# Performance work log

Hardware: AMD Instinct MI355X
Metric: run time of the kernel (lower is better)

## Reference

```python
import jax, jax.numpy as jnp
import numpy as np

DIM = 1024
D_STATE = 16
D_CONV = 4
EXPAND = 2
D_INNER = EXPAND * DIM
BATCH = 4
SEQ = 2048


def setup_inputs() -> dict:
    key = jax.random.key(0)
    ks = jax.random.split(key, 9)
    n = lambda i, shape, scale=0.02: (jax.random.normal(ks[i], shape, jnp.float32) * scale)
    return {
        "x": jax.random.normal(ks[0], (BATCH, SEQ, DIM), jnp.float32),
        "in_proj_w": n(1, (D_INNER, DIM)),
        "conv_w": n(2, (D_INNER, D_CONV), 0.1),          # depthwise kernel (groups=d_inner)
        "x_proj_w": n(3, (2 * D_STATE + 1, D_INNER)),
        "dt_proj_w": n(4, (D_INNER, 1), 1.0),
        "dt_proj_b": n(5, (D_INNER,), 0.1),
        "A_log": jax.random.normal(ks[6], (D_INNER, D_STATE), jnp.float32),
        "D": jnp.ones((D_INNER,), jnp.float32),
        "out_proj_w": n(7, (DIM, D_INNER)),
        "norm_w": jnp.ones((DIM,), jnp.float32),
        "norm_b": jnp.zeros((DIM,), jnp.float32),
    }


def reference(x, in_proj_w, conv_w, x_proj_w, dt_proj_w, dt_proj_b,
              A_log, D, out_proj_w, norm_w, norm_b):
    Bsz, L, _ = x.shape
    shortcut = x

    # LayerNorm
    mu = jnp.mean(x, axis=-1, keepdims=True)
    var = jnp.var(x, axis=-1, keepdims=True)
    h = (x - mu) / jnp.sqrt(var + 1e-5) * norm_w + norm_b

    # in_proj: [B,L,dim] -> [B,L,d_inner]
    h = h @ in_proj_w.T

    # causal depthwise conv1d (padding d_conv-1, truncate to L)
    hp = jnp.pad(h, ((0, 0), (D_CONV - 1, 0), (0, 0)))
    h_conv = sum(hp[:, k:k + L, :] * conv_w[:, k] for k in range(D_CONV))
    h = jax.nn.silu(h_conv)

    # x_proj -> dt (1), B (d_state), C (d_state)
    proj = h @ x_proj_w.T
    dt_in = proj[..., :1]
    B_param = proj[..., 1:1 + D_STATE]      # [B,L,d_state]
    C_param = proj[..., 1 + D_STATE:]       # [B,L,d_state]
    dt = jax.nn.softplus(dt_in @ dt_proj_w.T + dt_proj_b)  # [B,L,d_inner]

    A = -jnp.exp(A_log)                     # [d_inner, d_state]

    def step(state, inp):
        dt_t, B_t, C_t, x_t = inp           # [B,d_inner],[B,ds],[B,ds],[B,d_inner]
        state = jnp.exp(A[None] * dt_t[:, :, None]) * state \
                + B_t[:, None, :] * x_t[:, :, None]          # [B,d_inner,d_state]
        y = jnp.einsum('bnd,bd->bn', state, C_t) + D * x_t   # [B,d_inner]
        return state, y

    init = jnp.zeros((Bsz, D_INNER, D_STATE), x.dtype)
    xs = (jnp.swapaxes(dt, 0, 1), jnp.swapaxes(B_param, 0, 1),
          jnp.swapaxes(C_param, 0, 1), jnp.swapaxes(h, 0, 1))
    state, ys = jax.lax.scan(step, init, xs)
    y = jnp.swapaxes(ys, 0, 1)              # [B,L,d_inner]

    out = jax.nn.silu(y) @ out_proj_w.T + shortcut
    return out, state
```

## Files before the change

kernel.cpp:

```cpp
#include <hip/hip_runtime.h>

typedef unsigned short u16;
typedef unsigned int u32;
typedef __attribute__((ext_vector_type(8))) short short8;
typedef __attribute__((ext_vector_type(4))) float f32x4;
typedef __attribute__((ext_vector_type(8))) unsigned short ushort8_t;

#define SEQ 2048
#define DIM 1024
#define DINNER 2048
#define NPROJ 33
#define NPROJ_PAD 48
#define LC 64
#define NC 32

__device__ __forceinline__ u16 f2bf(float f) {
  union { float f; u32 u; } v; v.f = f;
  u32 r = (v.u + 0x7fffu + ((v.u >> 16) & 1u)) >> 16;
  return (u16)r;
}
__device__ __forceinline__ float bf2f(u16 s) {
  union { u32 u; float f; } v; v.u = ((u32)s) << 16;
  return v.f;
}
__device__ __forceinline__ float fexp2(float x) {
#if __has_builtin(__builtin_amdgcn_exp2f)
  return __builtin_amdgcn_exp2f(x);
#else
  return __expf(x * 0.69314718f);
#endif
}
__device__ __forceinline__ float softplus(float x) {
  return fmaxf(x, 0.f) + __logf(1.f + __expf(-fabsf(x)));
}
__device__ __forceinline__ void async16(const void* g, void* l) {
  __builtin_amdgcn_global_load_lds(
      (const __attribute__((address_space(1))) u32*)g,
      (__attribute__((address_space(3))) u32*)l, 16, 0, 0);
}

__global__ void cast_f2b_kernel(const float* __restrict__ src, u16* __restrict__ dst, int n4) {
  int i = blockIdx.x * 256 + threadIdx.x;
  if (i < n4) {
    float4 v = ((const float4*)src)[i];
    ushort4 o;
    o.x = f2bf(v.x); o.y = f2bf(v.y); o.z = f2bf(v.z); o.w = f2bf(v.w);
    ((ushort4*)dst)[i] = o;
  }
}

__global__ void cast_w2pad_kernel(const float* __restrict__ src, u16* __restrict__ dst) {
  int i = blockIdx.x * 256 + threadIdx.x;
  int j = i >> 11, k = i & 2047;
  dst[i] = (j < NPROJ) ? f2bf(src[j * 2048 + k]) : (u16)0;
}

__global__ __launch_bounds__(256) void ln_kernel(const float* __restrict__ x,
                                                 const float* __restrict__ w,
                                                 const float* __restrict__ b,
                                                 u16* __restrict__ h) {
  const int row = blockIdx.x;
  const int tid = threadIdx.x;
  const int lane = tid & 63, wave = tid >> 6;
  const float4 v = ((const float4*)(x + (size_t)row * DIM))[tid];
  float s = v.x + v.y + v.z + v.w;
  float q = v.x * v.x + v.y * v.y + v.z * v.z + v.w * v.w;
  for (int off = 32; off; off >>= 1) {
    s += __shfl_down(s, off);
    q += __shfl_down(q, off);
  }
  __shared__ float sbuf[8];
  if (lane == 0) { sbuf[wave] = s; sbuf[4 + wave] = q; }
  __syncthreads();
  float tot = sbuf[0] + sbuf[1] + sbuf[2] + sbuf[3];
  float totq = sbuf[4] + sbuf[5] + sbuf[6] + sbuf[7];
  const float mean = tot * (1.0f / DIM);
  const float var = totq * (1.0f / DIM) - mean * mean;
  const float rs = rsqrtf(var + 1e-5f);
  const float4 wv = ((const float4*)w)[tid];
  const float4 bv = ((const float4*)b)[tid];
  ushort4 o;
  o.x = f2bf((v.x - mean) * rs * wv.x + bv.x);
  o.y = f2bf((v.y - mean) * rs * wv.y + bv.y);
  o.z = f2bf((v.z - mean) * rs * wv.z + bv.z);
  o.w = f2bf((v.w - mean) * rs * wv.w + bv.w);
  ((ushort4*)(h + (size_t)row * DIM))[tid] = o;
}

__global__ __launch_bounds__(256) void gemm_bf16_kernel(const u16* __restrict__ A,
                                                        const u16* __restrict__ Bt,
                                                        u16* __restrict__ C,
                                                        int K, int N) {
  __shared__ u16 As[128 * 32];
  __shared__ u16 Bs[128 * 32];
  const int tid = threadIdx.x;
  const int lane = tid & 63, wave = tid >> 6;
  const int wm = wave >> 1, wn = wave & 1;
  const int row16 = lane & 15, quad = lane >> 4;
  const int bn = blockIdx.x, bm = blockIdx.y;
  f32x4 acc[4][4] = {};
  const u16* Ablk = A + (size_t)bm * 128 * K;
  const u16* Bblk = Bt + (size_t)bn * 128 * K;
  for (int k0 = 0; k0 < K; k0 += 32) {
#pragma unroll
    for (int i = 0; i < 2; ++i) {
      int c = tid + i * 256;
      int r = c >> 2, cc = (c & 3) * 8;
      async16(Ablk + (size_t)r * K + k0 + cc, &As[c * 8]);
      async16(Bblk + (size_t)r * K + k0 + cc, &Bs[c * 8]);
    }
    __syncthreads();
    short8 af[4], bfr[4];
#pragma unroll
    for (int i = 0; i < 4; ++i) {
      af[i] = *(const short8*)&As[(wm * 64 + i * 16 + row16) * 32 + quad * 8];
      bfr[i] = *(const short8*)&Bs[(wn * 64 + i * 16 + row16) * 32 + quad * 8];
    }
#pragma unroll
    for (int i = 0; i < 4; ++i)
#pragma unroll
      for (int j = 0; j < 4; ++j)
        acc[i][j] = __builtin_amdgcn_mfma_f32_16x16x32_bf16(af[i], bfr[j], acc[i][j], 0, 0, 0);
    __syncthreads();
  }
#pragma unroll
  for (int i = 0; i < 4; ++i) {
    int m = bm * 128 + wm * 64 + i * 16 + quad * 4;
#pragma unroll
    for (int j = 0; j < 4; ++j) {
      int n = bn * 128 + wn * 64 + j * 16 + row16;
#pragma unroll
      for (int r = 0; r < 4; ++r)
        C[(size_t)(m + r) * N + n] = f2bf(acc[i][j][r]);
    }
  }
}

__global__ __launch_bounds__(256) void gemm_out_kernel(const u16* __restrict__ A,
                                                       const u16* __restrict__ Bt,
                                                       const float* __restrict__ resid,
                                                       float* __restrict__ C,
                                                       int K, int N) {
  __shared__ u16 As[128 * 32];
  __shared__ u16 Bs[128 * 32];
  const int tid = threadIdx.x;
  const int lane = tid & 63, wave = tid >> 6;
  const int wm = wave >> 1, wn = wave & 1;
  const int row16 = lane & 15, quad = lane >> 4;
  const int bn = blockIdx.x, bm = blockIdx.y;
  f32x4 acc[4][4] = {};
  const u16* Ablk = A + (size_t)bm * 128 * K;
  const u16* Bblk = Bt + (size_t)bn * 128 * K;
  for (int k0 = 0; k0 < K; k0 += 32) {
#pragma unroll
    for (int i = 0; i < 2; ++i) {
      int c = tid + i * 256;
      int r = c >> 2, cc = (c & 3) * 8;
      async16(Ablk + (size_t)r * K + k0 + cc, &As[c * 8]);
      async16(Bblk + (size_t)r * K + k0 + cc, &Bs[c * 8]);
    }
    __syncthreads();
    short8 af[4], bfr[4];
#pragma unroll
    for (int i = 0; i < 4; ++i) {
      af[i] = *(const short8*)&As[(wm * 64 + i * 16 + row16) * 32 + quad * 8];
      bfr[i] = *(const short8*)&Bs[(wn * 64 + i * 16 + row16) * 32 + quad * 8];
    }
#pragma unroll
    for (int i = 0; i < 4; ++i)
#pragma unroll
      for (int j = 0; j < 4; ++j)
        acc[i][j] = __builtin_amdgcn_mfma_f32_16x16x32_bf16(af[i], bfr[j], acc[i][j], 0, 0, 0);
    __syncthreads();
  }
#pragma unroll
  for (int i = 0; i < 4; ++i) {
    int m = bm * 128 + wm * 64 + i * 16 + quad * 4;
#pragma unroll
    for (int j = 0; j < 4; ++j) {
      int n = bn * 128 + wn * 64 + j * 16 + row16;
#pragma unroll
      for (int r = 0; r < 4; ++r) {
        size_t idx = (size_t)(m + r) * N + n;
        C[idx] = acc[i][j][r] + resid[idx];
      }
    }
  }
}

__global__ __launch_bounds__(256) void conv_silu_kernel(const u16* __restrict__ c1,
                                                        const float* __restrict__ cw,
                                                        u16* __restrict__ cs) {
  const int tid = threadIdx.x;
  const int dg = tid * 8;
  const size_t m0 = (size_t)blockIdx.x * 8;
  const int l0 = (int)(m0 & (SEQ - 1));
  float w[4][8];
  {
    const float4* cw4 = (const float4*)(cw + (size_t)dg * 4);
#pragma unroll
    for (int c = 0; c < 8; ++c) {
      float4 v = cw4[c];
      w[0][c] = v.x; w[1][c] = v.y; w[2][c] = v.z; w[3][c] = v.w;
    }
  }
  const u16* base = c1 + m0 * DINNER + dg;
  ushort8_t win0, win1, win2, win3;
  const ushort8_t zero = (ushort8_t)0;
  if (l0 == 0) {
    win0 = zero; win1 = zero; win2 = zero;
  } else {
    win0 = *(const ushort8_t*)(base - 3 * DINNER);
    win1 = *(const ushort8_t*)(base - 2 * DINNER);
    win2 = *(const ushort8_t*)(base - 1 * DINNER);
  }
  win3 = *(const ushort8_t*)(base);
#pragma unroll
  for (int t = 0; t < 8; ++t) {
    ushort8_t nxt = win3;
    if (t < 7) nxt = *(const ushort8_t*)(base + (size_t)(t + 1) * DINNER);
    ushort8_t o;
#pragma unroll
    for (int c = 0; c < 8; ++c) {
      float acc = bf2f((u16)win0[c]) * w[0][c];
      acc = fmaf(bf2f((u16)win1[c]), w[1][c], acc);
      acc = fmaf(bf2f((u16)win2[c]), w[2][c], acc);
      acc = fmaf(bf2f((u16)win3[c]), w[3][c], acc);
      const float s = acc / (1.f + __expf(-acc));
      o[c] = (unsigned short)f2bf(s);
    }
    *(ushort8_t*)(cs + (m0 + t) * DINNER + dg) = o;
    win0 = win1; win1 = win2; win2 = win3; win3 = nxt;
  }
}

__global__ __launch_bounds__(256) void gemm_w2_kernel(const u16* __restrict__ A,
                                                      const u16* __restrict__ Bt,
                                                      float* __restrict__ C) {
  __shared__ u16 As[128 * 32];
  __shared__ u16 Bs[48 * 32];
  const int tid = threadIdx.x;
  const int lane = tid & 63, wave = tid >> 6;
  const int row16 = lane & 15, quad = lane >> 4;
  const int bm = blockIdx.x;
  const int K = DINNER;
  f32x4 acc[2][3] = {};
  const u16* Ablk = A + (size_t)bm * 128 * K;
  for (int k0 = 0; k0 < K; k0 += 32) {
#pragma unroll
    for (int i = 0; i < 2; ++i) {
      int c = tid + i * 256;
      int r = c >> 2, cc = (c & 3) * 8;
      async16(Ablk + (size_t)r * K + k0 + cc, &As[c * 8]);
    }
    if (tid < 192) {
      int c = tid;
      int r = c >> 2, cc = (c & 3) * 8;
      async16(Bt + (size_t)r * K + k0 + cc, &Bs[c * 8]);
    }
    __syncthreads();
    short8 af[2], bfr[3];
#pragma unroll
    for (int i = 0; i < 2; ++i)
      af[i] = *(const short8*)&As[(wave * 32 + i * 16 + row16) * 32 + quad * 8];
#pragma unroll
    for (int j = 0; j < 3; ++j)
      bfr[j] = *(const short8*)&Bs[(j * 16 + row16) * 32 + quad * 8];
#pragma unroll
    for (int i = 0; i < 2; ++i)
#pragma unroll
      for (int j = 0; j < 3; ++j)
        acc[i][j] = __builtin_amdgcn_mfma_f32_16x16x32_bf16(af[i], bfr[j], acc[i][j], 0, 0, 0);
    __syncthreads();
  }
#pragma unroll
  for (int i = 0; i < 2; ++i) {
    int m = bm * 128 + wave * 32 + i * 16 + quad * 4;
#pragma unroll
    for (int j = 0; j < 3; ++j) {
      int n = j * 16 + row16;
#pragma unroll
      for (int r = 0; r < 4; ++r)
        C[(size_t)(m + r) * NPROJ_PAD + n] = acc[i][j][r];
    }
  }
}

__global__ __launch_bounds__(256) void scan_phase1(const float* __restrict__ proj,
                                                   const u16* __restrict__ xs,
                                                   const float* __restrict__ dtw_,
                                                   const float* __restrict__ dtb_,
                                                   const float* __restrict__ A_log,
                                                   float* __restrict__ S,
                                                   float* __restrict__ Tdt) {
  __shared__ float Bs[LC][16];
  __shared__ float DTin[LC];
  const int tid = threadIdx.x;
  const int d = blockIdx.x * 256 + tid;
  const int c = blockIdx.y;
  const int b = blockIdx.z;
  const size_t mrow = (size_t)b * SEQ + c * LC;
  for (int i = tid; i < LC * 16; i += 256) {
    int t = i >> 4, n = i & 15;
    Bs[t][n] = proj[(mrow + t) * NPROJ_PAD + 1 + n];
  }
  if (tid < LC) DTin[tid] = proj[(mrow + tid) * NPROJ_PAD];
  __syncthreads();
  float An2[16];
#pragma unroll
  for (int n = 0; n < 16; ++n) An2[n] = -__expf(A_log[d * 16 + n]) * 1.44269504f;
  const float dtw = dtw_[d], dtb = dtb_[d];
  float s[16];
#pragma unroll
  for (int n = 0; n < 16; ++n) s[n] = 0.f;
  float Tsum = 0.f;
  const u16* xp = xs + mrow * DINNER + d;
  u16 xnext = *xp;
#pragma unroll 2
  for (int t = 0; t < LC; ++t) {
    const float xv = bf2f(xnext);
    if (t + 1 < LC) xnext = xp[(size_t)(t + 1) * DINNER];
    const float sp = softplus(fmaf(DTin[t], dtw, dtb));
    Tsum += sp;
    const float4 B0 = *(const float4*)&Bs[t][0];
    const float4 B1 = *(const float4*)&Bs[t][4];
    const float4 B2 = *(const float4*)&Bs[t][8];
    const float4 B3 = *(const float4*)&Bs[t][12];
    const float bb[16] = {B0.x, B0.y, B0.z, B0.w, B1.x, B1.y, B1.z, B1.w,
                          B2.x, B2.y, B2.z, B2.w, B3.x, B3.y, B3.z, B3.w};
#pragma unroll
    for (int n = 0; n < 16; ++n)
      s[n] = fmaf(fexp2(An2[n] * sp), s[n], bb[n] * xv);
  }
  const size_t so = ((size_t)(b * NC + c) * DINNER + d) * 16;
#pragma unroll
  for (int n4 = 0; n4 < 4; ++n4)
    *(float4*)(S + so + n4 * 4) = make_float4(s[n4 * 4], s[n4 * 4 + 1], s[n4 * 4 + 2], s[n4 * 4 + 3]);
  Tdt[(size_t)(b * NC + c) * DINNER + d] = Tsum;
}

__global__ __launch_bounds__(256) void scan_phase2(const float* __restrict__ A_log,
                                                   float* __restrict__ S,
                                                   const float* __restrict__ Tdt,
                                                   float* __restrict__ out_state) {
  const int idx = blockIdx.x * 256 + threadIdx.x;
  const int b = idx >> 11, d = idx & (DINNER - 1);
  float An2[16];
#pragma unroll
  for (int n = 0; n < 16; ++n) An2[n] = -__expf(A_log[d * 16 + n]) * 1.44269504f;
  float prev[16];
#pragma unroll
  for (int n = 0; n < 16; ++n) prev[n] = 0.f;
  for (int c = 0; c < NC; ++c) {
    const size_t so = ((size_t)(b * NC + c) * DINNER + d) * 16;
    const float T = Tdt[(size_t)(b * NC + c) * DINNER + d];
    float loc[16];
#pragma unroll
    for (int n4 = 0; n4 < 4; ++n4) {
      float4 v = *(const float4*)(S + so + n4 * 4);
      loc[n4 * 4] = v.x; loc[n4 * 4 + 1] = v.y; loc[n4 * 4 + 2] = v.z; loc[n4 * 4 + 3] = v.w;
    }
#pragma unroll
    for (int n4 = 0; n4 < 4; ++n4)
      *(float4*)(S + so + n4 * 4) =
          make_float4(prev[n4 * 4], prev[n4 * 4 + 1], prev[n4 * 4 + 2], prev[n4 * 4 + 3]);
#pragma unroll
    for (int n = 0; n < 16; ++n)
      prev[n] = fmaf(fexp2(An2[n] * T), prev[n], loc[n]);
  }
#pragma unroll
  for (int n4 = 0; n4 < 4; ++n4)
    *(float4*)(out_state + ((size_t)b * DINNER + d) * 16 + n4 * 4) =
        make_float4(prev[n4 * 4], prev[n4 * 4 + 1], prev[n4 * 4 + 2], prev[n4 * 4 + 3]);
}

__global__ __launch_bounds__(256) void scan_phase3(const float* __restrict__ proj,
                                                   const u16* __restrict__ xs,
                                                   const float* __restrict__ dtw_,
                                                   const float* __restrict__ dtb_,
                                                   const float* __restrict__ A_log,
                                                   const float* __restrict__ Dp,
                                                   const float* __restrict__ S,
                                                   u16* __restrict__ ysil) {
  __shared__ float Bs[LC][16];
  __shared__ float Cs[LC][16];
  __shared__ float DTin[LC];
  const int tid = threadIdx.x;
  const int d = blockIdx.x * 256 + tid;
  const int c = blockIdx.y;
  const int b = blockIdx.z;
  const size_t mrow = (size_t)b * SEQ + c * LC;
  for (int i = tid; i < LC * 16; i += 256) {
    int t = i >> 4, n = i & 15;
    Bs[t][n] = proj[(mrow + t) * NPROJ_PAD + 1 + n];
    Cs[t][n] = proj[(mrow + t) * NPROJ_PAD + 17 + n];
  }
  if (tid < LC) DTin[tid] = proj[(mrow + tid) * NPROJ_PAD];
  __syncthreads();
  float An2[16];
#pragma unroll
  for (int n = 0; n < 16; ++n) An2[n] = -__expf(A_log[d * 16 + n]) * 1.44269504f;
  const float dtw = dtw_[d], dtb = dtb_[d], Dd = Dp[d];
  float s[16];
  const size_t so = ((size_t)(b * NC + c) * DINNER + d) * 16;
#pragma unroll
  for (int n4 = 0; n4 < 4; ++n4) {
    float4 v = *(const float4*)(S + so + n4 * 4);
    s[n4 * 4] = v.x; s[n4 * 4 + 1] = v.y; s[n4 * 4 + 2] = v.z; s[n4 * 4 + 3] = v.w;
  }
  const u16* xp = xs + mrow * DINNER + d;
  u16* yp = ysil + mrow * DINNER + d;
  u16 xnext = *xp;
#pragma unroll 2
  for (int t = 0; t < LC; ++t) {
    const float xv = bf2f(xnext);
    if (t + 1 < LC) xnext = xp[(size_t)(t + 1) * DINNER];
    const float sp = softplus(fmaf(DTin[t], dtw, dtb));
    const float4 B0 = *(const float4*)&Bs[t][0];
    const float4 B1 = *(const float4*)&Bs[t][4];
    const float4 B2 = *(const float4*)&Bs[t][8];
    const float4 B3 = *(const float4*)&Bs[t][12];
    const float bb[16] = {B0.x, B0.y, B0.z, B0.w, B1.x, B1.y, B1.z, B1.w,
                          B2.x, B2.y, B2.z, B2.w, B3.x, B3.y, B3.z, B3.w};
#pragma unroll
    for (int n = 0; n < 16; ++n)
      s[n] = fmaf(fexp2(An2[n] * sp), s[n], bb[n] * xv);
    const float4 C0 = *(const float4*)&Cs[t][0];
    const float4 C1 = *(const float4*)&Cs[t][4];
    const float4 C2 = *(const float4*)&Cs[t][8];
    const float4 C3 = *(const float4*)&Cs[t][12];
    const float cc[16] = {C0.x, C0.y, C0.z, C0.w, C1.x, C1.y, C1.z, C1.w,
                          C2.x, C2.y, C2.z, C2.w, C3.x, C3.y, C3.z, C3.w};
    float y = Dd * xv;
#pragma unroll
    for (int n = 0; n < 16; ++n) y = fmaf(cc[n], s[n], y);
    const float sy = y / (1.f + __expf(-y));
    yp[(size_t)t * DINNER] = f2bf(sy);
  }
}

extern "C" void kernel_launch(void* const* d_in, const int* in_sizes, int n_in,
                              void* d_out, int out_size, void* d_ws, size_t ws_size,
                              hipStream_t stream) {
  const float* x = (const float*)d_in[0];
  const float* in_proj_w = (const float*)d_in[1];
  const float* conv_w = (const float*)d_in[2];
  const float* x_proj_w = (const float*)d_in[3];
  const float* dt_proj_w = (const float*)d_in[4];
  const float* dt_proj_b = (const float*)d_in[5];
  const float* A_log = (const float*)d_in[6];
  const float* Dvec = (const float*)d_in[7];
  const float* out_proj_w = (const float*)d_in[8];
  const float* norm_w = (const float*)d_in[9];
  const float* norm_b = (const float*)d_in[10];

  char* ws = (char*)d_ws;
  u16* h = (u16*)(ws + 0);
  u16* w1b = (u16*)(ws + 16777216);
  u16* w3b = (u16*)(ws + 20971520);
  u16* w2b = (u16*)(ws + 25165824);
  u16* c1 = (u16*)(ws + 25362432);
  u16* ysil = c1;
  u16* cs = (u16*)(ws + 58916864);
  float* proj = (float*)(ws + 92471296);
  float* Sbuf = (float*)(ws + 94044160);
  float* Tdt = (float*)(ws + 110821376);

  float* out = (float*)d_out;
  float* out_state = out + (size_t)4 * SEQ * DIM;

  cast_f2b_kernel<<<2048, 256, 0, stream>>>(in_proj_w, w1b, DINNER * DIM / 4);
  cast_f2b_kernel<<<2048, 256, 0, stream>>>(out_proj_w, w3b, DIM * DINNER / 4);
  cast_w2pad_kernel<<<384, 256, 0, stream>>>(x_proj_w, w2b);
  ln_kernel<<<8192, 256, 0, stream>>>(x, norm_w, norm_b, h);
  gemm_bf16_kernel<<<dim3(DINNER / 128, 64), 256, 0, stream>>>(h, w1b, c1, DIM, DINNER);
  conv_silu_kernel<<<1024, 256, 0, stream>>>(c1, conv_w, cs);
  gemm_w2_kernel<<<64, 256, 0, stream>>>(cs, w2b, proj);
  scan_phase1<<<dim3(DINNER / 256, NC, 4), 256, 0, stream>>>(proj, cs, dt_proj_w, dt_proj_b,
                                                             A_log, Sbuf, Tdt);
  scan_phase2<<<32, 256, 0, stream>>>(A_log, Sbuf, Tdt, out_state);
  scan_phase3<<<dim3(DINNER / 256, NC, 4), 256, 0, stream>>>(proj, cs, dt_proj_w, dt_proj_b,
                                                             A_log, Dvec, Sbuf, ysil);
  gemm_out_kernel<<<dim3(DIM / 128, 64), 256, 0, stream>>>(ysil, w3b, x, out, DINNER, DIM);
}
```

Measured before the change: 424.7 us.

## Halve scan chunk length, store chunk states in bf16, widen phase2, fuse weight casts

Scan chunks shrink from 64 to 32 steps, doubling chunk count so phases 1 and 3 run more blocks with shorter serial loops. Inter-chunk states are stored as bf16, halving S buffer traffic. Phase 2 is parallelised across state-dimension quarters, giving four times as many threads. The two weight-cast launches are merged into one. The bf16 state carry adds rounding error to the recurrence and the final state, and phase 2 now walks twice as many chunks serially.

```diff
diff --git a/kernel.cpp b/kernel.cpp
--- a/kernel.cpp
+++ b/kernel.cpp
@@ -11,8 +11,8 @@
 #define DINNER 2048
 #define NPROJ 33
 #define NPROJ_PAD 48
-#define LC 64
-#define NC 32
+#define LC 32
+#define NC 64
 
 __device__ __forceinline__ u16 f2bf(float f) {
   union { float f; u32 u; } v; v.f = f;
@@ -39,14 +39,16 @@
       (__attribute__((address_space(3))) u32*)l, 16, 0, 0);
 }
 
-__global__ void cast_f2b_kernel(const float* __restrict__ src, u16* __restrict__ dst, int n4) {
+__global__ void cast_w_kernel(const float* __restrict__ w1, const float* __restrict__ w3,
+                              u16* __restrict__ o1, u16* __restrict__ o3) {
   int i = blockIdx.x * 256 + threadIdx.x;
-  if (i < n4) {
-    float4 v = ((const float4*)src)[i];
-    ushort4 o;
-    o.x = f2bf(v.x); o.y = f2bf(v.y); o.z = f2bf(v.z); o.w = f2bf(v.w);
-    ((ushort4*)dst)[i] = o;
-  }
+  float4 a = ((const float4*)w1)[i];
+  float4 b = ((const float4*)w3)[i];
+  ushort4 oa, ob;
+  oa.x = f2bf(a.x); oa.y = f2bf(a.y); oa.z = f2bf(a.z); oa.w = f2bf(a.w);
+  ob.x = f2bf(b.x); ob.y = f2bf(b.y); ob.z = f2bf(b.z); ob.w = f2bf(b.w);
+  ((ushort4*)o1)[i] = oa;
+  ((ushort4*)o3)[i] = ob;
 }
 
 __global__ void cast_w2pad_kernel(const float* __restrict__ src, u16* __restrict__ dst) {
@@ -286,12 +288,13 @@
   }
 }
 
+
 __global__ __launch_bounds__(256) void scan_phase1(const float* __restrict__ proj,
                                                    const u16* __restrict__ xs,
                                                    const float* __restrict__ dtw_,
                                                    const float* __restrict__ dtb_,
                                                    const float* __restrict__ A_log,
-                                                   float* __restrict__ S,
+                                                   u16* __restrict__ S,
                                                    float* __restrict__ Tdt) {
   __shared__ float Bs[LC][16];
   __shared__ float DTin[LC];
@@ -333,45 +336,47 @@
       s[n] = fmaf(fexp2(An2[n] * sp), s[n], bb[n] * xv);
   }
   const size_t so = ((size_t)(b * NC + c) * DINNER + d) * 16;
-#pragma unroll
-  for (int n4 = 0; n4 < 4; ++n4)
-    *(float4*)(S + so + n4 * 4) = make_float4(s[n4 * 4], s[n4 * 4 + 1], s[n4 * 4 + 2], s[n4 * 4 + 3]);
+  ushort8_t o0, o1;
+#pragma unroll
+  for (int j = 0; j < 8; ++j) {
+    o0[j] = (unsigned short)f2bf(s[j]);
+    o1[j] = (unsigned short)f2bf(s[8 + j]);
+  }
+  *(ushort8_t*)(S + so) = o0;
+  *(ushort8_t*)(S + so + 8) = o1;
   Tdt[(size_t)(b * NC + c) * DINNER + d] = Tsum;
 }
 
 __global__ __launch_bounds__(256) void scan_phase2(const float* __restrict__ A_log,
-                                                   float* __restrict__ S,
+                                                   u16* __restrict__ S,
                                                    const float* __restrict__ Tdt,
                                                    float* __restrict__ out_state) {
   const int idx = blockIdx.x * 256 + threadIdx.x;
-  const int b = idx >> 11, d = idx & (DINNER - 1);
-  float An2[16];
-#pragma unroll
-  for (int n = 0; n < 16; ++n) An2[n] = -__expf(A_log[d * 16 + n]) * 1.44269504f;
-  float prev[16];
-#pragma unroll
-  for (int n = 0; n < 16; ++n) prev[n] = 0.f;
+  const int nq = idx & 3;
+  const int d = (idx >> 2) & (DINNER - 1);
+  const int b = idx >> 13;
+  float An2[4];
+#pragma unroll
+  for (int n = 0; n < 4; ++n) An2[n] = -__expf(A_log[d * 16 + nq * 4 + n]) * 1.44269504f;
+  float prev[4] = {0.f, 0.f, 0.f, 0.f};
   for (int c = 0; c < NC; ++c) {
-    const size_t so = ((size_t)(b * NC + c) * DINNER + d) * 16;
-    const float T = Tdt[(size_t)(b * NC + c) * DINNER + d];
-    float loc[16];
-#pragma unroll
-    for (int n4 = 0; n4 < 4; ++n4) {
-      float4 v = *(const float4*)(S + so + n4 * 4);
-      loc[n4 * 4] = v.x; loc[n4 * 4 + 1] = v.y; loc[n4 * 4 + 2] = v.z; loc[n4 * 4 + 3] = v.w;
-    }
-#pragma unroll
-    for (int n4 = 0; n4 < 4; ++n4)
-      *(float4*)(S + so + n4 * 4) =
-          make_float4(prev[n4 * 4], prev[n4 * 4 + 1], prev[n4 * 4 + 2], prev[n4 * 4 + 3]);
-#pragma unroll
-    for (int n = 0; n < 16; ++n)
-      prev[n] = fmaf(fexp2(An2[n] * T), prev[n], loc[n]);
-  }
-#pragma unroll
-  for (int n4 = 0; n4 < 4; ++n4)
-    *(float4*)(out_state + ((size_t)b * DINNER + d) * 16 + n4 * 4) =
-        make_float4(prev[n4 * 4], prev[n4 * 4 + 1], prev[n4 * 4 + 2], prev[n4 * 4 + 3]);
+    const size_t base = (size_t)(b * NC + c) * DINNER + d;
+    const float T = Tdt[base];
+    const size_t so = base * 16 + nq * 4;
+    ushort4 lv = *(const ushort4*)(S + so);
+    const float loc[4] = {bf2f(lv.x), bf2f(lv.y), bf2f(lv.z), bf2f(lv.w)};
+    ushort4 pv;
+    pv.x = f2bf(prev[0]); pv.y = f2bf(prev[1]); pv.z = f2bf(prev[2]); pv.w = f2bf(prev[3]);
+    *(ushort4*)(S + so) = pv;
+    const float dk = fexp2(An2[0] * T), dk1 = fexp2(An2[1] * T);
+    const float dk2 = fexp2(An2[2] * T), dk3 = fexp2(An2[3] * T);
+    prev[0] = fmaf(dk, prev[0], loc[0]);
+    prev[1] = fmaf(dk1, prev[1], loc[1]);
+    prev[2] = fmaf(dk2, prev[2], loc[2]);
+    prev[3] = fmaf(dk3, prev[3], loc[3]);
+  }
+  *(float4*)(out_state + ((size_t)b * DINNER + d) * 16 + nq * 4) =
+      make_float4(prev[0], prev[1], prev[2], prev[3]);
 }
 
 __global__ __launch_bounds__(256) void scan_phase3(const float* __restrict__ proj,
@@ -380,7 +385,7 @@
                                                    const float* __restrict__ dtb_,
                                                    const float* __restrict__ A_log,
                                                    const float* __restrict__ Dp,
-                                                   const float* __restrict__ S,
+                                                   const u16* __restrict__ S,
                                                    u16* __restrict__ ysil) {
   __shared__ float Bs[LC][16];
   __shared__ float Cs[LC][16];
@@ -403,10 +408,14 @@
   const float dtw = dtw_[d], dtb = dtb_[d], Dd = Dp[d];
   float s[16];
   const size_t so = ((size_t)(b * NC + c) * DINNER + d) * 16;
-#pragma unroll
-  for (int n4 = 0; n4 < 4; ++n4) {
-    float4 v = *(const float4*)(S + so + n4 * 4);
-    s[n4 * 4] = v.x; s[n4 * 4 + 1] = v.y; s[n4 * 4 + 2] = v.z; s[n4 * 4 + 3] = v.w;
+  {
+    ushort8_t v0 = *(const ushort8_t*)(S + so);
+    ushort8_t v1 = *(const ushort8_t*)(S + so + 8);
+#pragma unroll
+    for (int j = 0; j < 8; ++j) {
+      s[j] = bf2f((u16)v0[j]);
+      s[8 + j] = bf2f((u16)v1[j]);
+    }
   }
   const u16* xp = xs + mrow * DINNER + d;
   u16* yp = ysil + mrow * DINNER + d;
@@ -463,14 +472,13 @@
   u16* ysil = c1;
   u16* cs = (u16*)(ws + 58916864);
   float* proj = (float*)(ws + 92471296);
-  float* Sbuf = (float*)(ws + 94044160);
+  u16* Sbuf = (u16*)(ws + 94044160);
   float* Tdt = (float*)(ws + 110821376);
 
   float* out = (float*)d_out;
   float* out_state = out + (size_t)4 * SEQ * DIM;
 
-  cast_f2b_kernel<<<2048, 256, 0, stream>>>(in_proj_w, w1b, DINNER * DIM / 4);
-  cast_f2b_kernel<<<2048, 256, 0, stream>>>(out_proj_w, w3b, DIM * DINNER / 4);
+  cast_w_kernel<<<2048, 256, 0, stream>>>(in_proj_w, out_proj_w, w1b, w3b);
   cast_w2pad_kernel<<<384, 256, 0, stream>>>(x_proj_w, w2b);
   ln_kernel<<<8192, 256, 0, stream>>>(x, norm_w, norm_b, h);
   gemm_bf16_kernel<<<dim3(DINNER / 128, 64), 256, 0, stream>>>(h, w1b, c1, DIM, DINNER);
@@ -478,7 +486,7 @@
   gemm_w2_kernel<<<64, 256, 0, stream>>>(cs, w2b, proj);
   scan_phase1<<<dim3(DINNER / 256, NC, 4), 256, 0, stream>>>(proj, cs, dt_proj_w, dt_proj_b,
                                                              A_log, Sbuf, Tdt);
-  scan_phase2<<<32, 256, 0, stream>>>(A_log, Sbuf, Tdt, out_state);
+  scan_phase2<<<128, 256, 0, stream>>>(A_log, Sbuf, Tdt, out_state);
   scan_phase3<<<dim3(DINNER / 256, NC, 4), 256, 0, stream>>>(proj, cs, dt_proj_w, dt_proj_b,
                                                              A_log, Dvec, Sbuf, ysil);
   gemm_out_kernel<<<dim3(DIM / 128, 64), 256, 0, stream>>>(ysil, w3b, x, out, DINNER, DIM);
```

After: 395.4 us. -6.9%, faster.
